# Optimization experiments

Hardware: AMD Instinct MI355X
Metric: run time of the kernel (lower is better)

Reference implementation:

```python
import jax, jax.numpy as jnp
import numpy as np

GROUPS = 32
N_HEADS = 16
EPS = 1e-5


def setup_inputs() -> dict:
    key = jax.random.key(0)
    ks = jax.random.split(key, 5)
    b, c, t = 4, 1024, 1024
    return {
        "x": jax.random.normal(ks[0], (b, c, t), dtype=jnp.float32),
        "gn_weight": jnp.ones((c,), dtype=jnp.float32),
        "gn_bias": jnp.zeros((c,), dtype=jnp.float32),
        "qkv_w": jax.random.normal(ks[1], (3 * c, c), dtype=jnp.float32) * (c ** -0.5),
        "qkv_b": jax.random.normal(ks[2], (3 * c,), dtype=jnp.float32) * 0.02,
        "proj_w": jax.random.normal(ks[3], (c, c), dtype=jnp.float32) * (c ** -0.5),
        "proj_b": jax.random.normal(ks[4], (c,), dtype=jnp.float32) * 0.02,
    }


def _group_norm(x, weight, bias):
    # x: [b, c, t]; GroupNorm32 computes stats in float32 (already fp32 here)
    b, c, t = x.shape
    xg = x.reshape(b, GROUPS, c // GROUPS, t)
    mean = xg.mean(axis=(2, 3), keepdims=True)
    var = xg.var(axis=(2, 3), keepdims=True)
    xn = ((xg - mean) * jax.lax.rsqrt(var + EPS)).reshape(b, c, t)
    return xn * weight[None, :, None] + bias[None, :, None]


def reference(x, gn_weight, gn_bias, qkv_w, qkv_b, proj_w, proj_b):
    b, c, t = x.shape
    xn = _group_norm(x, gn_weight, gn_bias)
    # 1x1 Conv1d == channel matmul: [3c, c] x [b, c, t] -> [b, 3c, t]
    qkv = jnp.einsum('oc,bct->bot', qkv_w, xn) + qkv_b[None, :, None]
    ch = c // N_HEADS
    # legacy per-head interleaved layout: reshape to [b*H, 3*ch, t], split
    qkv = qkv.reshape(b * N_HEADS, 3 * ch, t)
    q, k, v = qkv[:, :ch], qkv[:, ch:2 * ch], qkv[:, 2 * ch:]
    scale = ch ** -0.25  # 1/sqrt(sqrt(ch)), applied to both q and k
    weight = jnp.einsum('bct,bcs->bts', q * scale, k * scale)  # [b*H, t, t]
    weight = jax.nn.softmax(weight.astype(jnp.float32), axis=-1).astype(weight.dtype)
    a = jnp.einsum('bts,bcs->bct', weight, v).reshape(b, c, t)
    h = jnp.einsum('oc,bct->bot', proj_w, a) + proj_b[None, :, None]
    return x + h
```

## Files before the change

### kernel.cpp

```cpp
#include <hip/hip_runtime.h>
#include <hip/hip_bf16.h>

typedef __bf16 bf16;
typedef __bf16 bf16x2 __attribute__((ext_vector_type(2)));
typedef __bf16 bf16x4 __attribute__((ext_vector_type(4)));
typedef __bf16 bf16x8 __attribute__((ext_vector_type(8)));
typedef float  f32x4  __attribute__((ext_vector_type(4)));
typedef float  f32x16 __attribute__((ext_vector_type(16)));

static __device__ __forceinline__ f32x4 mfma16(bf16x8 a, bf16x8 b, f32x4 c) {
  return __builtin_amdgcn_mfma_f32_16x16x32_bf16(a, b, c, 0, 0, 0);
}
static __device__ __forceinline__ f32x16 mfma32(bf16x8 a, bf16x8 b, f32x16 c) {
  return __builtin_amdgcn_mfma_f32_32x32x16_bf16(a, b, c, 0, 0, 0);
}

static __device__ __forceinline__ void gload_lds16(const bf16* g, bf16* l) {
  __builtin_amdgcn_global_load_lds(
      (const __attribute__((address_space(1))) void*)g,
      (__attribute__((address_space(3))) void*)l, 16, 0, 0);
}

static __device__ __forceinline__ int cvtpk(float lo, float hi) {
  int w;
  asm("v_cvt_pk_bf16_f32 %0, %1, %2" : "=v"(w) : "v"(lo), "v"(hi));
  return w;
}
static __device__ __forceinline__ void plswap(int& x, int& y) {
  asm("v_permlane32_swap_b32 %0, %1" : "+v"(x), "+v"(y));
}

#define VMCNT0() asm volatile("s_waitcnt vmcnt(0)" ::: "memory")
#define BARRIER()                                        \
  do {                                                   \
    asm volatile("" ::: "memory");                       \
    __builtin_amdgcn_s_barrier();                        \
    asm volatile("" ::: "memory");                       \
  } while (0)

__global__ __launch_bounds__(512) void pre_kernel(const float* __restrict__ x,
                                                  const float* __restrict__ gw,
                                                  const float* __restrict__ gb,
                                                  bf16* __restrict__ xnT,
                                                  const float* __restrict__ qkv_w,
                                                  bf16* __restrict__ wq,
                                                  const float* __restrict__ proj_w,
                                                  bf16* __restrict__ wp) {
  int blk = blockIdx.x;
  int tid = threadIdx.x;
  if (blk >= 512) {
    int i = (blk - 512) * 512 + tid;
    const int na4 = 3072 * 1024 / 4;
    const float* src; bf16* dst;
    if (i < na4) { src = qkv_w; dst = wq; }
    else         { src = proj_w; dst = wp; i -= na4; }
    float4 v = ((const float4*)src)[i];
    bf16x4 o = { (bf16)v.x, (bf16)v.y, (bf16)v.z, (bf16)v.w };
    *(bf16x4*)(dst + 4ll * i) = o;
    return;
  }
  int id = blk;
  int b = id >> 7, g = (id >> 2) & 31, qtr = id & 3;
  const float* xb = x + ((size_t)b * 1024 + g * 32) * 1024;
  float s = 0.f, sq = 0.f;
  const float4* x4 = (const float4*)xb;
  for (int i = tid; i < 8192; i += 512) {
    float4 v = x4[i];
    s  += v.x + v.y + v.z + v.w;
    sq += v.x * v.x + v.y * v.y + v.z * v.z + v.w * v.w;
  }
#pragma unroll
  for (int off = 32; off; off >>= 1) { s += __shfl_down(s, off); sq += __shfl_down(sq, off); }
  __shared__ float red[16];
  int wv = tid >> 6;
  if ((tid & 63) == 0) { red[wv] = s; red[8 + wv] = sq; }
  __syncthreads();
  s = 0.f; sq = 0.f;
#pragma unroll
  for (int i = 0; i < 8; ++i) { s += red[i]; sq += red[8 + i]; }
  float mean = s * (1.f / 32768.f);
  float var  = sq * (1.f / 32768.f) - mean * mean;
  float rstd = rsqrtf(var + 1e-5f);

  __shared__ bf16 tile[64][36];
  int c = tid >> 4, q = tid & 15;
  int r = tid >> 3, q2 = tid & 7;
  float wc = gw[g * 32 + c] * rstd;
  float fb = gb[g * 32 + c] - mean * wc;
  for (int t0 = qtr * 256; t0 < qtr * 256 + 256; t0 += 64) {
    float4 v = *(const float4*)(xb + (size_t)c * 1024 + t0 + q * 4);
    tile[q * 4 + 0][c] = (bf16)(v.x * wc + fb);
    tile[q * 4 + 1][c] = (bf16)(v.y * wc + fb);
    tile[q * 4 + 2][c] = (bf16)(v.z * wc + fb);
    tile[q * 4 + 3][c] = (bf16)(v.w * wc + fb);
    __syncthreads();
    *(bf16x4*)&xnT[((size_t)b * 1024 + t0 + r) * 1024 + g * 32 + q2 * 4] =
        *(bf16x4*)&tile[r][q2 * 4];
    __syncthreads();
  }
}

__global__ __launch_bounds__(512, 2) void qkv_kernel(
    const bf16* __restrict__ A, const bf16* __restrict__ Bw,
    const float* __restrict__ bias,
    bf16* __restrict__ qkT, bf16* __restrict__ vC) {
  extern __shared__ __align__(16) bf16 smem[];

  int tid = threadIdx.x, wid = tid >> 6, lane = tid & 63;
  int l15 = lane & 15, l4 = lane >> 4;
  int wr = wid >> 2, wc = wid & 3;
  int rsw = (l15 & 7) << 4;

  int sid = (blockIdx.x & 7) * 64 + (blockIdx.x >> 3);
  int bx = sid & 15, by = (sid >> 4) & 7, z = sid >> 7;
  int m0 = by * 128, n0 = bx * 192;
  const bf16* Ab = A + (size_t)z * 1024 * 1024 + (size_t)m0 * 1024;
  const bf16* Bb = Bw + (size_t)n0 * 1024;

  int srow = tid >> 3;
  int csw  = (tid & 7) ^ (srow & 7);
  auto stageA = [&](int d, int kt) {
    bf16* dst = smem + d * 8192;
    const bf16* src = Ab + kt * 64 + csw * 8;
#pragma unroll
    for (int L = 0; L < 2; ++L)
      gload_lds16(src + (size_t)(L * 64 + srow) * 1024, dst + (L * 512 + wid * 64) * 8);
  };
  auto stageB = [&](int d, int kt) {
    bf16* dst = smem + 16384 + d * 12288;
    const bf16* src = Bb + kt * 64 + csw * 8;
#pragma unroll
    for (int L = 0; L < 3; ++L)
      gload_lds16(src + (size_t)(L * 64 + srow) * 1024, dst + (L * 512 + wid * 64) * 8);
  };

  f32x4 acc[4][3] = {};

  auto compute = [&](int d) {
    const char* Ab8 = (const char*)smem + d * 16384 + wr * 8192;
    const char* Bb8 = (const char*)smem + 32768 + d * 24576;
    bf16x8 bfr[3][2], af[4][2];
#pragma unroll
    for (int ni = 0; ni < 3; ++ni) {
      int rb = (wc * 48 + ni * 16 + l15) * 128;
#pragma unroll
      for (int kk = 0; kk < 2; ++kk)
        bfr[ni][kk] = *(const bf16x8*)(Bb8 + rb + ((kk * 64 + l4 * 16) ^ rsw));
    }
#pragma unroll
    for (int mi = 0; mi < 4; ++mi) {
      int rb = (mi * 16 + l15) * 128;
#pragma unroll
      for (int kk = 0; kk < 2; ++kk)
        af[mi][kk] = *(const bf16x8*)(Ab8 + rb + ((kk * 64 + l4 * 16) ^ rsw));
    }
#pragma unroll
    for (int mi = 0; mi < 4; ++mi)
#pragma unroll
      for (int ni = 0; ni < 3; ++ni)
#pragma unroll
        for (int kk = 0; kk < 2; ++kk)
          acc[mi][ni] = mfma16(af[mi][kk], bfr[ni][kk], acc[mi][ni]);
  };

  stageA(0, 0); stageB(0, 0);
  VMCNT0();
  BARRIER();

  for (int t = 0; t < 16; ++t) {
    int d = t & 1;
    if (t < 15) { stageB(d ^ 1, t + 1); stageA(d ^ 1, t + 1); }
    compute(d);
    VMCNT0();
    BARRIER();
  }

  const float scale = 0.35355339059327373f;
  int h = bx;
#pragma unroll
  for (int ni = 0; ni < 3; ++ni) {
    int oin = wc * 48 + ni * 16;
    float bv = bias[n0 + oin + l15];
#pragma unroll
    for (int mi = 0; mi < 4; ++mi) {
      int tb = m0 + wr * 64 + mi * 16 + l4 * 4;
      f32x4 v = acc[mi][ni];
      if (oin < 128) {
#pragma unroll
        for (int i = 0; i < 4; ++i)
          qkT[((size_t)z * 1024 + tb + i) * 2048 + h * 128 + oin + l15] =
              (bf16)((v[i] + bv) * scale);
      } else {
        bf16x4 st = { (bf16)(v[0] + bv), (bf16)(v[1] + bv),
                      (bf16)(v[2] + bv), (bf16)(v[3] + bv) };
        *(bf16x4*)&vC[(((size_t)z * 16 + h) * 64 + (oin - 128 + l15)) * 1024 + tb] = st;
      }
    }
  }
}

#define VMCNT2() asm volatile("s_waitcnt vmcnt(2)" ::: "memory")
__global__ __launch_bounds__(512, 1) void proj_kernel(
    const bf16* __restrict__ A, const bf16* __restrict__ Bw,
    const float* __restrict__ bias,
    const float* __restrict__ xres, float* __restrict__ out) {
  extern __shared__ __align__(16) bf16 smem[];

  int tid = threadIdx.x, wid = tid >> 6, lane = tid & 63;
  int l15 = lane & 15, l4 = lane >> 4;
  int wr = wid >> 2, wc = wid & 3;
  int rsw = (l15 & 7) << 4;

  int sid = (blockIdx.x & 7) * 32 + (blockIdx.x >> 3);
  int bx = sid & 7, by = (sid >> 3) & 7, z = sid >> 6;
  int m0 = by * 128, n0 = bx * 128;
  const bf16* Ab = A + (size_t)z * 1024 * 1024 + (size_t)m0 * 1024;
  const bf16* Bb = Bw + (size_t)n0 * 1024;

  int srow = tid >> 3;
  int csw  = (tid & 7) ^ (srow & 7);
  auto stageA = [&](int d, int kt) {
    bf16* dst = smem + d * 8192;
    const bf16* src = Ab + kt * 64 + csw * 8;
#pragma unroll
    for (int L = 0; L < 2; ++L)
      gload_lds16(src + (size_t)(L * 64 + srow) * 1024, dst + (L * 512 + wid * 64) * 8);
  };
  auto stageB = [&](int d, int kt) {
    bf16* dst = smem + 24576 + d * 8192;
    const bf16* src = Bb + kt * 64 + csw * 8;
#pragma unroll
    for (int L = 0; L < 2; ++L)
      gload_lds16(src + (size_t)(L * 64 + srow) * 1024, dst + (L * 512 + wid * 64) * 8);
  };

  f32x4 acc[4][2] = {};

  auto compute = [&](int ta, int tb) {
    const char* Ab8 = (const char*)smem + ta * 16384 + wr * 8192;
    const char* Bb8 = (const char*)smem + 49152 + tb * 16384;
    bf16x8 bfr[2][2], af[4][2];
#pragma unroll
    for (int ni = 0; ni < 2; ++ni) {
      int rb = (wc * 32 + ni * 16 + l15) * 128;
#pragma unroll
      for (int kk = 0; kk < 2; ++kk)
        bfr[ni][kk] = *(const bf16x8*)(Bb8 + rb + ((kk * 64 + l4 * 16) ^ rsw));
    }
#pragma unroll
    for (int mi = 0; mi < 4; ++mi) {
      int rb = (mi * 16 + l15) * 128;
#pragma unroll
      for (int kk = 0; kk < 2; ++kk)
        af[mi][kk] = *(const bf16x8*)(Ab8 + rb + ((kk * 64 + l4 * 16) ^ rsw));
    }
#pragma unroll
    for (int mi = 0; mi < 4; ++mi)
#pragma unroll
      for (int ni = 0; ni < 2; ++ni)
#pragma unroll
        for (int kk = 0; kk < 2; ++kk)
          acc[mi][ni] = mfma16(af[mi][kk], bfr[ni][kk], acc[mi][ni]);
  };

  stageA(0, 0); stageB(0, 0); stageA(1, 1);
  VMCNT2();
  BARRIER();

  for (int t = 0; t < 14; ++t) {
    stageB((t + 1) & 1, t + 1);
    stageA((t + 2) % 3, t + 2);
    compute(t % 3, t & 1);
    VMCNT2();
    BARRIER();
  }
  stageB(1, 15);
  compute(2, 0);
  VMCNT0();
  BARRIER();
  compute(0, 1);

#pragma unroll
  for (int ni = 0; ni < 2; ++ni) {
    int o = n0 + wc * 32 + ni * 16 + l15;
    float bv = bias[o];
#pragma unroll
    for (int mi = 0; mi < 4; ++mi) {
      int tb = m0 + wr * 64 + mi * 16 + l4 * 4;
      size_t base = ((size_t)z * 1024 + o) * 1024 + tb;
      float4 xr = *(const float4*)(xres + base);
      f32x4 v = acc[mi][ni];
      float4 ov = { xr.x + v[0] + bv, xr.y + v[1] + bv,
                    xr.z + v[2] + bv, xr.w + v[3] + bv };
      *(float4*)(out + base) = ov;
    }
  }
}

__global__ __launch_bounds__(256, 3) void attn_kernel(const bf16* __restrict__ qkT,
                                                      const bf16* __restrict__ vC,
                                                      bf16* __restrict__ aT) {
  __shared__ __align__(16) bf16 Kt[2][64 * 64];
  __shared__ __align__(16) bf16 Vt[2][64 * 64];

  int id = blockIdx.x;
  int sid = (id & 7) * 64 + (id >> 3);
  int head = sid >> 3, tblk = sid & 7;
  int b = head >> 4, h = head & 15;
  int t0 = tblk * 128;
  int tid = threadIdx.x, wid = tid >> 6, lane = tid & 63;
  int l31 = lane & 31, hi = lane >> 5;
  int trow = t0 + wid * 32;

  const bf16* kbase = qkT + (size_t)b * 1024 * 2048 + h * 128 + 64;
  const bf16* vbase = vC + (size_t)(b * 16 + h) * 64 * 1024;
  int rsw = (lane & 7) << 4;

  const bf16* qrow = qkT + ((size_t)b * 1024 + trow + l31) * 2048 + h * 128;
  bf16x8 qf[4];
#pragma unroll
  for (int kb = 0; kb < 4; ++kb) qf[kb] = *(const bf16x8*)(qrow + kb * 16 + hi * 8);

  int rl = lane >> 3;
  int scol = (((lane & 7) * 16) ^ (rl << 4)) >> 1;
  auto stage = [&](int buf, int st) {
    int s0 = st * 64;
#pragma unroll
    for (int j = 0; j < 2; ++j) {
      int g8 = wid * 2 + j;
      int r = g8 * 8 + rl;
      gload_lds16(kbase + (size_t)(s0 + r) * 2048 + scol, &Kt[buf][g8 * 512]);
      gload_lds16(vbase + (size_t)r * 1024 + s0 + scol, &Vt[buf][g8 * 512]);
    }
  };

  float m_run = -1e30f, l_run = 0.f;
  f32x16 oacc[2] = {};

  stage(0, 0);
  __syncthreads();

  for (int st = 0; st < 16; ++st) {
    int cur = st & 1;
    if (st < 15) stage(cur ^ 1, st + 1);

    const char* Kb = (const char*)Kt[cur];
    f32x16 sf[2] = {};
    __builtin_amdgcn_s_setprio(1);
#pragma unroll
    for (int sb = 0; sb < 2; ++sb) {
      int rowb = (sb * 32 + l31) * 128;
#pragma unroll
      for (int kb = 0; kb < 4; ++kb) {
        bf16x8 kf = *(const bf16x8*)(Kb + rowb + ((kb * 32 + hi * 16) ^ rsw));
        sf[sb] = mfma32(kf, qf[kb], sf[sb]);
      }
    }
    __builtin_amdgcn_s_setprio(0);

    float mb;
    {
      float m0v = fmaxf(sf[0][0], sf[0][1]);
#pragma unroll
      for (int r = 2; r < 16; ++r) m0v = fmaxf(m0v, sf[0][r]);
#pragma unroll
      for (int r = 0; r < 16; ++r) m0v = fmaxf(m0v, sf[1][r]);
      mb = m0v;
    }
    mb = fmaxf(mb, __shfl_xor(mb, 32));
    if (!__all(mb - m_run <= 8.f)) {
      float mn = fmaxf(m_run, mb);
      float corr = __expf(m_run - mn);
      m_run = mn;
      l_run *= corr;
#pragma unroll
      for (int cb = 0; cb < 2; ++cb)
#pragma unroll
        for (int r = 0; r < 16; ++r) oacc[cb][r] *= corr;
    }

    float sbsum = 0.f;
    bf16x8 pf[4];
#pragma unroll
    for (int sb = 0; sb < 2; ++sb) {
      float p[16];
#pragma unroll
      for (int r = 0; r < 16; ++r) {
        p[r] = __expf(sf[sb][r] - m_run);
        sbsum += p[r];
      }
      int w0 = cvtpk(p[0], p[1]),   w1 = cvtpk(p[2], p[3]);
      int w2 = cvtpk(p[4], p[5]),   w3 = cvtpk(p[6], p[7]);
      int w4 = cvtpk(p[8], p[9]),   w5 = cvtpk(p[10], p[11]);
      int w6 = cvtpk(p[12], p[13]), w7 = cvtpk(p[14], p[15]);
      plswap(w0, w2); plswap(w1, w3);
      plswap(w4, w6); plswap(w5, w7);
      int4 f0 = { w0, w1, w2, w3 };
      int4 f1 = { w4, w5, w6, w7 };
      pf[sb * 2 + 0] = *(bf16x8*)&f0;
      pf[sb * 2 + 1] = *(bf16x8*)&f1;
    }
    sbsum += __shfl_xor(sbsum, 32);
    l_run += sbsum;

    const char* Vb = (const char*)Vt[cur];
    __builtin_amdgcn_s_setprio(1);
#pragma unroll
    for (int ks = 0; ks < 4; ++ks) {
#pragma unroll
      for (int cb = 0; cb < 2; ++cb) {
        bf16x8 vf = *(const bf16x8*)(Vb + (cb * 32 + l31) * 128 + ((ks * 32 + hi * 16) ^ rsw));
        oacc[cb] = mfma32(vf, pf[ks], oacc[cb]);
      }
    }
    __builtin_amdgcn_s_setprio(0);
    __syncthreads();
  }

  float rdiv = 1.f / l_run;
  int t = trow + l31;
#pragma unroll
  for (int cb = 0; cb < 2; ++cb) {
#pragma unroll
    for (int q = 0; q < 4; ++q) {
      bf16x4 ov = { (bf16)(oacc[cb][q * 4 + 0] * rdiv), (bf16)(oacc[cb][q * 4 + 1] * rdiv),
                    (bf16)(oacc[cb][q * 4 + 2] * rdiv), (bf16)(oacc[cb][q * 4 + 3] * rdiv) };
      int c0 = h * 64 + cb * 32 + hi * 4 + q * 8;
      *(bf16x4*)&aT[((size_t)b * 1024 + t) * 1024 + c0] = ov;
    }
  }
}

extern "C" void kernel_launch(void* const* d_in, const int* in_sizes, int n_in,
                              void* d_out, int out_size, void* d_ws, size_t ws_size,
                              hipStream_t stream) {
  const float* x      = (const float*)d_in[0];
  const float* gw     = (const float*)d_in[1];
  const float* gb     = (const float*)d_in[2];
  const float* qkv_w  = (const float*)d_in[3];
  const float* qkv_b  = (const float*)d_in[4];
  const float* proj_w = (const float*)d_in[5];
  const float* proj_b = (const float*)d_in[6];
  float* out = (float*)d_out;

  char* ws = (char*)d_ws;
  bf16* wq_bf = (bf16*)(ws);
  bf16* wp_bf = (bf16*)(ws + 6ll  * 1024 * 1024);
  bf16* xnT   = (bf16*)(ws + 8ll  * 1024 * 1024);
  bf16* qkT   = (bf16*)(ws + 16ll * 1024 * 1024);
  bf16* vC    = (bf16*)(ws + 32ll * 1024 * 1024);
  bf16* aT    = (bf16*)(ws + 40ll * 1024 * 1024);

  hipFuncSetAttribute(reinterpret_cast<const void*>(qkv_kernel),
                      hipFuncAttributeMaxDynamicSharedMemorySize, 81920);
  hipFuncSetAttribute(reinterpret_cast<const void*>(proj_kernel),
                      hipFuncAttributeMaxDynamicSharedMemorySize, 81920);

  pre_kernel<<<dim3(2560), dim3(512), 0, stream>>>(x, gw, gb, xnT, qkv_w, wq_bf, proj_w, wp_bf);
  qkv_kernel<<<dim3(512), dim3(512), 81920, stream>>>(xnT, wq_bf, qkv_b, qkT, vC);
  attn_kernel<<<dim3(512), dim3(256), 0, stream>>>(qkT, vC, aT);
  proj_kernel<<<dim3(256), dim3(512), 81920, stream>>>(aT, wp_bf, proj_b, x, out);
}
```

Measured before the change: 93.93 us.

## Halve proj tile width to double block count and occupancy

The projection GEMM tile goes from 128x128 to 128x64. The grid doubles to 512 blocks, launch bounds allow 2 blocks per CU, and LDS drops to 48KB. The three-stage A / two-stage B pipeline with vmcnt(2) is replaced by a simple double buffer that waits for all loads every iteration. This aims to fill all CUs on the 256-CU part and raise occupancy, at the cost of more A reloads and a less overlapped load schedule.

```diff
diff --git a/kernel.cpp b/kernel.cpp
--- a/kernel.cpp
+++ b/kernel.cpp
@@ -199,8 +199,7 @@
   }
 }
 
-#define VMCNT2() asm volatile("s_waitcnt vmcnt(2)" ::: "memory")
-__global__ __launch_bounds__(512, 1) void proj_kernel(
+__global__ __launch_bounds__(512, 2) void proj_kernel(
     const bf16* __restrict__ A, const bf16* __restrict__ Bw,
     const float* __restrict__ bias,
     const float* __restrict__ xres, float* __restrict__ out) {
@@ -211,9 +210,9 @@
   int wr = wid >> 2, wc = wid & 3;
   int rsw = (l15 & 7) << 4;
 
-  int sid = (blockIdx.x & 7) * 32 + (blockIdx.x >> 3);
-  int bx = sid & 7, by = (sid >> 3) & 7, z = sid >> 6;
-  int m0 = by * 128, n0 = bx * 128;
+  int sid = (blockIdx.x & 7) * 64 + (blockIdx.x >> 3);
+  int bx = sid & 15, by = (sid >> 4) & 7, z = sid >> 7;
+  int m0 = by * 128, n0 = bx * 64;
   const bf16* Ab = A + (size_t)z * 1024 * 1024 + (size_t)m0 * 1024;
   const bf16* Bb = Bw + (size_t)n0 * 1024;
 
@@ -227,26 +226,21 @@
       gload_lds16(src + (size_t)(L * 64 + srow) * 1024, dst + (L * 512 + wid * 64) * 8);
   };
   auto stageB = [&](int d, int kt) {
-    bf16* dst = smem + 24576 + d * 8192;
+    bf16* dst = smem + 16384 + d * 4096;
     const bf16* src = Bb + kt * 64 + csw * 8;
-#pragma unroll
-    for (int L = 0; L < 2; ++L)
-      gload_lds16(src + (size_t)(L * 64 + srow) * 1024, dst + (L * 512 + wid * 64) * 8);
-  };
-
-  f32x4 acc[4][2] = {};
-
-  auto compute = [&](int ta, int tb) {
-    const char* Ab8 = (const char*)smem + ta * 16384 + wr * 8192;
-    const char* Bb8 = (const char*)smem + 49152 + tb * 16384;
-    bf16x8 bfr[2][2], af[4][2];
-#pragma unroll
-    for (int ni = 0; ni < 2; ++ni) {
-      int rb = (wc * 32 + ni * 16 + l15) * 128;
-#pragma unroll
-      for (int kk = 0; kk < 2; ++kk)
-        bfr[ni][kk] = *(const bf16x8*)(Bb8 + rb + ((kk * 64 + l4 * 16) ^ rsw));
-    }
+    gload_lds16(src + (size_t)srow * 1024, dst + (wid * 64) * 8);
+  };
+
+  f32x4 acc[4] = {};
+
+  auto compute = [&](int d) {
+    const char* Ab8 = (const char*)smem + d * 16384 + wr * 8192;
+    const char* Bb8 = (const char*)smem + 32768 + d * 8192;
+    bf16x8 bfr[2], af[4][2];
+    int rbB = (wc * 16 + l15) * 128;
+#pragma unroll
+    for (int kk = 0; kk < 2; ++kk)
+      bfr[kk] = *(const bf16x8*)(Bb8 + rbB + ((kk * 64 + l4 * 16) ^ rsw));
 #pragma unroll
     for (int mi = 0; mi < 4; ++mi) {
       int rb = (mi * 16 + l15) * 128;
@@ -257,43 +251,33 @@
 #pragma unroll
     for (int mi = 0; mi < 4; ++mi)
 #pragma unroll
-      for (int ni = 0; ni < 2; ++ni)
-#pragma unroll
-        for (int kk = 0; kk < 2; ++kk)
-          acc[mi][ni] = mfma16(af[mi][kk], bfr[ni][kk], acc[mi][ni]);
-  };
-
-  stageA(0, 0); stageB(0, 0); stageA(1, 1);
-  VMCNT2();
-  BARRIER();
-
-  for (int t = 0; t < 14; ++t) {
-    stageB((t + 1) & 1, t + 1);
-    stageA((t + 2) % 3, t + 2);
-    compute(t % 3, t & 1);
-    VMCNT2();
-    BARRIER();
-  }
-  stageB(1, 15);
-  compute(2, 0);
+      for (int kk = 0; kk < 2; ++kk)
+        acc[mi] = mfma16(af[mi][kk], bfr[kk], acc[mi]);
+  };
+
+  stageA(0, 0); stageB(0, 0);
   VMCNT0();
   BARRIER();
-  compute(0, 1);
-
-#pragma unroll
-  for (int ni = 0; ni < 2; ++ni) {
-    int o = n0 + wc * 32 + ni * 16 + l15;
-    float bv = bias[o];
-#pragma unroll
-    for (int mi = 0; mi < 4; ++mi) {
-      int tb = m0 + wr * 64 + mi * 16 + l4 * 4;
-      size_t base = ((size_t)z * 1024 + o) * 1024 + tb;
-      float4 xr = *(const float4*)(xres + base);
-      f32x4 v = acc[mi][ni];
-      float4 ov = { xr.x + v[0] + bv, xr.y + v[1] + bv,
-                    xr.z + v[2] + bv, xr.w + v[3] + bv };
-      *(float4*)(out + base) = ov;
-    }
+
+  for (int t = 0; t < 16; ++t) {
+    int d = t & 1;
+    if (t < 15) { stageB(d ^ 1, t + 1); stageA(d ^ 1, t + 1); }
+    compute(d);
+    VMCNT0();
+    BARRIER();
+  }
+
+  int o = n0 + wc * 16 + l15;
+  float bv = bias[o];
+#pragma unroll
+  for (int mi = 0; mi < 4; ++mi) {
+    int tb = m0 + wr * 64 + mi * 16 + l4 * 4;
+    size_t base = ((size_t)z * 1024 + o) * 1024 + tb;
+    float4 xr = *(const float4*)(xres + base);
+    f32x4 v = acc[mi];
+    float4 ov = { xr.x + v[0] + bv, xr.y + v[1] + bv,
+                  xr.z + v[2] + bv, xr.w + v[3] + bv };
+    *(float4*)(out + base) = ov;
   }
 }
 
@@ -454,10 +438,10 @@
   hipFuncSetAttribute(reinterpret_cast<const void*>(qkv_kernel),
                       hipFuncAttributeMaxDynamicSharedMemorySize, 81920);
   hipFuncSetAttribute(reinterpret_cast<const void*>(proj_kernel),
-                      hipFuncAttributeMaxDynamicSharedMemorySize, 81920);
+                      hipFuncAttributeMaxDynamicSharedMemorySize, 49152);
 
   pre_kernel<<<dim3(2560), dim3(512), 0, stream>>>(x, gw, gb, xnT, qkv_w, wq_bf, proj_w, wp_bf);
   qkv_kernel<<<dim3(512), dim3(512), 81920, stream>>>(xnT, wq_bf, qkv_b, qkT, vC);
   attn_kernel<<<dim3(512), dim3(256), 0, stream>>>(qkT, vC, aT);
-  proj_kernel<<<dim3(256), dim3(512), 81920, stream>>>(aT, wp_bf, proj_b, x, out);
-}
+  proj_kernel<<<dim3(512), dim3(512), 49152, stream>>>(aT, wp_bf, proj_b, x, out);
+}
```

New measurement: 93.05 us. Within noise of the previous version (-0.9%).
